# Optimization experiments

Measured on AMD Instinct MI355X. Metric: run time of the kernel, lower is better.

Reference implementation:

```python
import jax, jax.numpy as jnp
import numpy as np

B_, L_, D_ = 4, 4096, 256
EXPAND = 2
DI_ = EXPAND * D_      # 512 inner channels
H_ = 8                 # heads
P_ = DI_ // H_         # 64 head dim
N_ = 16                # d_state
K_ = 3                 # depthwise conv kernel


def setup_inputs() -> dict:
    key = jax.random.key(0)
    ks = jax.random.split(key, 32)

    def n(i, shape, s=0.02):
        return jax.random.normal(ks[i], shape, jnp.float32) * s

    inp = {"inputs": jax.random.normal(ks[0], (B_, L_, D_), jnp.float32)}
    i = 1
    for pre in ("f_", "b_"):
        inp[pre + "in_proj_w"] = n(i, (2 * DI_, D_)); i += 1
        inp[pre + "in_proj_b"] = jnp.zeros((2 * DI_,), jnp.float32)
        inp[pre + "x_proj_w"] = n(i, (DI_ + 2 * H_ * N_, DI_)); i += 1
        inp[pre + "x_proj_b"] = jnp.zeros((DI_ + 2 * H_ * N_,), jnp.float32)
        inp[pre + "dt_bias"] = jnp.full((DI_,), -4.0, jnp.float32)  # softplus -> small dt
        inp[pre + "A_log"] = jnp.log(jnp.tile(jnp.arange(1, N_ + 1, dtype=jnp.float32), (DI_, 1)))
        inp[pre + "D_skip"] = jnp.ones((DI_,), jnp.float32)
        inp[pre + "out_proj_w"] = n(i, (D_, DI_)); i += 1
        inp[pre + "out_proj_b"] = jnp.zeros((D_,), jnp.float32)
    inp["norm_w"] = jnp.ones((D_,), jnp.float32)
    inp["norm_b"] = jnp.zeros((D_,), jnp.float32)
    inp["conv_w"] = n(20, (D_, 1, K_), 0.1)   # depthwise: (out_ch, in_ch/groups=1, k)
    inp["conv_b"] = jnp.zeros((D_,), jnp.float32)
    return inp


def _layernorm(x, w, b):
    m = x.mean(-1, keepdims=True)
    v = ((x - m) ** 2).mean(-1, keepdims=True)
    return (x - m) * jax.lax.rsqrt(v + 1e-5) * w + b


def _mh_ssm(x, in_w, in_b, xp_w, xp_b, dt_b, A_log, D_skip, out_w, out_b):
    # Multihead selective-scan SSM (Mamba-style). x: (B, L, D)
    Bsz, L, _ = x.shape
    xz = x @ in_w.T + in_b                      # (B, L, 2*DI)
    xi, z = jnp.split(xz, 2, axis=-1)
    xi = jax.nn.silu(xi)                        # (B, L, DI)
    proj = xi @ xp_w.T + xp_b                   # (B, L, DI + 2*H*N)
    dt = jax.nn.softplus(proj[..., :DI_] + dt_b)        # (B, L, DI)
    Bm = proj[..., DI_:DI_ + H_ * N_].reshape(Bsz, L, H_, N_)
    Cm = proj[..., DI_ + H_ * N_:].reshape(Bsz, L, H_, N_)
    A = -jnp.exp(A_log).reshape(H_, P_, N_)     # (H, P, N), negative
    x4 = xi.reshape(Bsz, L, H_, P_)
    dt4 = dt.reshape(Bsz, L, H_, P_)

    def step(h, t):
        xt, dtt, Bt, Ct = t                     # (B,H,P), (B,H,P), (B,H,N), (B,H,N)
        dA = jnp.exp(dtt[..., None] * A)        # (B,H,P,N)
        h = h * dA + dtt[..., None] * Bt[:, :, None, :] * xt[..., None]
        y = jnp.einsum('bhpn,bhn->bhp', h, Ct)
        return h, y

    xs = (x4.transpose(1, 0, 2, 3), dt4.transpose(1, 0, 2, 3),
          Bm.transpose(1, 0, 2, 3), Cm.transpose(1, 0, 2, 3))
    h0 = jnp.zeros((Bsz, H_, P_, N_), x.dtype)
    _, ys = jax.lax.scan(step, h0, xs)          # ys: (L,B,H,P)
    y = ys.transpose(1, 0, 2, 3).reshape(Bsz, L, DI_) + xi * D_skip
    y = y * jax.nn.silu(z)                      # gating
    return y @ out_w.T + out_b                  # (B, L, D)


def reference(inputs,
              f_in_proj_w, f_in_proj_b, f_x_proj_w, f_x_proj_b, f_dt_bias,
              f_A_log, f_D_skip, f_out_proj_w, f_out_proj_b,
              b_in_proj_w, b_in_proj_b, b_x_proj_w, b_x_proj_b, b_dt_bias,
              b_A_log, b_D_skip, b_out_proj_w, b_out_proj_b,
              norm_w, norm_b, conv_w, conv_b):
    # Cascaded bidirectional SSM: backward(flip(norm(forward(x)))) then flip back
    y1 = _mh_ssm(inputs, f_in_proj_w, f_in_proj_b, f_x_proj_w, f_x_proj_b,
                 f_dt_bias, f_A_log, f_D_skip, f_out_proj_w, f_out_proj_b)
    y1n = jnp.flip(_layernorm(y1, norm_w, norm_b), axis=1)
    y2 = _mh_ssm(y1n, b_in_proj_w, b_in_proj_b, b_x_proj_w, b_x_proj_b,
                 b_dt_bias, b_A_log, b_D_skip, b_out_proj_w, b_out_proj_b)
    out = jnp.flip(y2, axis=1)
    # locality branch: depthwise Conv1d (groups=C) + exact GELU
    xt = inputs.transpose(0, 2, 1)              # (B, C, L)
    c = jax.lax.conv_general_dilated(
        xt, conv_w, window_strides=(1,), padding=[(1, 1)],
        dimension_numbers=('NCH', 'OIH', 'NCH'), feature_group_count=D_)
    c = jax.nn.gelu(c + conv_b[None, :, None], approximate=False)
    return out + c.transpose(0, 2, 1)
```

## Files before the change

kernel.cpp:

```cpp
#include <hip/hip_runtime.h>
#include <hip/hip_bf16.h>
#include <cstdint>
#include <cstddef>

#define B_  4
#define L_  4096
#define D_  256
#define DI_ 512
#define H_  8
#define P_  64
#define N_  16
#define M_  (B_ * L_)
#define PROJ_ (DI_ + 2 * H_ * N_)

#define NC_ 128
#define CL_ (L_ / NC_)
#define NSEQ_ (B_ * H_ * P_ * N_)
#define LOG2E_ 1.4426950408889634f

typedef __bf16 bf16x8 __attribute__((ext_vector_type(8)));
typedef float f32x4 __attribute__((ext_vector_type(4)));

__device__ __forceinline__ void cp16_lds(const __hip_bfloat16* g, short* lds) {
    __builtin_amdgcn_global_load_lds(
        (const __attribute__((address_space(1))) void*)g,
        (__attribute__((address_space(3))) void*)lds, 16, 0, 0);
}
__device__ __forceinline__ void cp16f_lds(const float* g, float* lds) {
    __builtin_amdgcn_global_load_lds(
        (const __attribute__((address_space(1))) void*)g,
        (__attribute__((address_space(3))) void*)lds, 16, 0, 0);
}

#define FS0 (M_ * D_)
#define FS1 (2 * DI_ * D_)
#define FS2 (PROJ_ * DI_)
#define FS3 (D_ * DI_)
#define FC1 (FS0 + FS1)
#define FC2 (FC1 + FS2)
#define FC3 (FC2 + FS3)
#define FC4 (FC3 + FS1)
#define FC5 (FC4 + FS2)
#define FC6 (FC5 + FS3)

__launch_bounds__(256)
__global__ void f2b_all(const float* __restrict__ i0, const float* __restrict__ i1,
                        const float* __restrict__ i2, const float* __restrict__ i3,
                        const float* __restrict__ i4, const float* __restrict__ i5,
                        const float* __restrict__ i6,
                        __hip_bfloat16* o0, __hip_bfloat16* o1, __hip_bfloat16* o2,
                        __hip_bfloat16* o3, __hip_bfloat16* o4, __hip_bfloat16* o5,
                        __hip_bfloat16* o6) {
    for (int idx = blockIdx.x * 256 + threadIdx.x; idx < FC6; idx += gridDim.x * 256) {
        const float* s; __hip_bfloat16* d; int off;
        if (idx < FS0)      { s = i0; d = o0; off = idx; }
        else if (idx < FC1) { s = i1; d = o1; off = idx - FS0; }
        else if (idx < FC2) { s = i2; d = o2; off = idx - FC1; }
        else if (idx < FC3) { s = i3; d = o3; off = idx - FC2; }
        else if (idx < FC4) { s = i4; d = o4; off = idx - FC3; }
        else if (idx < FC5) { s = i5; d = o5; off = idx - FC4; }
        else                { s = i6; d = o6; off = idx - FC5; }
        d[off] = __float2bfloat16(s[off]);
    }
}

template <int EPI>
__launch_bounds__(256)
__global__ void gemm_mfma(const __hip_bfloat16* __restrict__ A,
                          const __hip_bfloat16* __restrict__ W,
                          const float* __restrict__ bias, int Kv,
                          float* __restrict__ out0, float* __restrict__ out1,
                          __hip_bfloat16* __restrict__ obf,
                          const float* __restrict__ aux,
                          const float* __restrict__ cw,
                          const float* __restrict__ cb,
                          const float* __restrict__ cinp) {
    __shared__ short As[128 * 64];
    __shared__ short Bs[128 * 64];
    const int tid = threadIdx.x;
    const int lane = tid & 63;
    const int wave = tid >> 6;
    const int bm = blockIdx.x * 128;
    const int bn = blockIdx.y * 128;
    const int wm = (wave >> 1) * 64;
    const int wn = (wave & 1) * 64;

    f32x4 acc[4][4];
#pragma unroll
    for (int i = 0; i < 4; ++i)
#pragma unroll
        for (int j = 0; j < 4; ++j) acc[i][j] = (f32x4)0.f;

    const int srow = lane >> 3;
    const int ssegx = ((lane & 7) ^ srow) * 8;
    const __hip_bfloat16* gA0 = A + (size_t)(bm + wave * 32 + srow) * Kv + ssegx;
    const __hip_bfloat16* gB0 = W + (size_t)(bn + wave * 32 + srow) * Kv + ssegx;
    short* lA0 = As + (wave * 32) * 64;
    short* lB0 = Bs + (wave * 32) * 64;

    const int fr = lane & 15;
    const int kq = lane >> 4;

    for (int k0 = 0; k0 < Kv; k0 += 64) {
#pragma unroll
        for (int rb = 0; rb < 4; ++rb) {
            cp16_lds(gA0 + (size_t)(rb * 8) * Kv + k0, lA0 + rb * 8 * 64);
            cp16_lds(gB0 + (size_t)(rb * 8) * Kv + k0, lB0 + rb * 8 * 64);
        }
        __syncthreads();
#pragma unroll
        for (int ks = 0; ks < 2; ++ks) {
            const int kgg = ks * 4 + kq;
            const int kslot = (kgg ^ (fr & 7)) * 8;
            bf16x8 af[4], bv[4];
#pragma unroll
            for (int i = 0; i < 4; ++i)
                af[i] = *reinterpret_cast<const bf16x8*>(
                    &As[(wm + i * 16 + fr) * 64 + kslot]);
#pragma unroll
            for (int j = 0; j < 4; ++j)
                bv[j] = *reinterpret_cast<const bf16x8*>(
                    &Bs[(wn + j * 16 + fr) * 64 + kslot]);
#pragma unroll
            for (int i = 0; i < 4; ++i)
#pragma unroll
                for (int j = 0; j < 4; ++j)
                    acc[i][j] = __builtin_amdgcn_mfma_f32_16x16x32_bf16(
                        af[i], bv[j], acc[i][j], 0, 0, 0);
        }
        __syncthreads();
    }

    const int n16 = lane & 15;
    const int r4 = (lane >> 4) * 4;
#pragma unroll
    for (int i = 0; i < 4; ++i) {
#pragma unroll
        for (int j = 0; j < 4; ++j) {
            const int cg = bn + wn + j * 16 + n16;
            const float bb = bias[cg];
#pragma unroll
            for (int v = 0; v < 4; ++v) {
                const int r = bm + wm + i * 16 + r4 + v;
                float val = acc[i][j][v] + bb;
                if (EPI == 0) {
                    out0[(size_t)r * 256 + cg] = val;
                } else if (EPI == 1) {
                    if (cg < DI_) {
                        val = val / (1.f + __expf(-val));
                        obf[(size_t)r * DI_ + cg] = __float2bfloat16(val);
                    } else {
                        out1[(size_t)r * DI_ + cg - DI_] = val;
                    }
                } else if (EPI == 2) {
                    if (cg < DI_) {
                        const float x = val + aux[cg];
                        val = (x > 20.f) ? x : __logf(1.f + __expf(x));
                    }
                    out0[(size_t)r * PROJ_ + cg] = val;
                } else {
                    const int b = r >> 12;
                    const int l = r & (L_ - 1);
                    const int lo = L_ - 1 - l;
                    const size_t base = ((size_t)(b << 12) + lo) * 256 + cg;
                    float cv = fmaf(cinp[base], cw[cg * 3 + 1], cb[cg]);
                    if (lo > 0) cv = fmaf(cinp[base - 256], cw[cg * 3 + 0], cv);
                    if (lo + 1 < L_) cv = fmaf(cinp[base + 256], cw[cg * 3 + 2], cv);
                    const float g = 0.5f * cv * (1.f + erff(cv * 0.70710678118654752f));
                    out0[base] = val + g;
                }
            }
        }
    }
}


__device__ __forceinline__ bool a_is_arith(const float* A2) {
    bool ok = true;
#pragma unroll
    for (int n = 1; n < N_; ++n)
        ok = ok && (fabsf(A2[n] - (float)(n + 1) * A2[0]) <= 1e-4f * fabsf(A2[n]));
    return ok;
}

__launch_bounds__(256)
__global__ void scan_chunk_state(const __hip_bfloat16* __restrict__ xi,
                                 const float* __restrict__ proj,
                                 const float* __restrict__ A_log,
                                 float* __restrict__ st_prod,
                                 float* __restrict__ st_hend) {
    __shared__ float bsh[4][CL_][16];
    const int bh = blockIdx.x;
    const int b = bh >> 3;
    const int h = bh & 7;
    const int lane = threadIdx.x & 63;
    const int wave = threadIdx.x >> 6;
    const int chunk = blockIdx.y * 4 + wave;
    const int t0 = chunk * CL_;
    const int c = h * P_ + lane;
    const int bOff = DI_ + h * N_;

    {
        const int stp = lane >> 2;
        const int off4 = (lane & 3) * 4;
        const float* base = proj + ((size_t)b * L_ + t0) * PROJ_ + bOff + off4;
#pragma unroll
        for (int r = 0; r < 2; ++r)
            cp16f_lds(base + (size_t)(r * 16 + stp) * PROJ_,
                      &bsh[wave][0][0] + r * 256);
    }

    float A2[N_], hs[N_];
#pragma unroll
    for (int n = 0; n < N_; ++n) {
        A2[n] = -__expf(A_log[c * N_ + n]) * LOG2E_;
        hs[n] = 0.f;
    }
    const bool fast = a_is_arith(A2);
    __syncthreads();

    const float* pDt = proj + ((size_t)b * L_ + t0) * PROJ_ + c;
    const __hip_bfloat16* px = xi + ((size_t)b * L_ + t0) * DI_ + c;
    float S = 0.f;

    if (fast) {
        float dtb[2][4], xb[2][4];
#pragma unroll
        for (int i = 0; i < 4; ++i) {
            dtb[0][i] = pDt[(size_t)i * PROJ_];
            xb[0][i] = __bfloat162float(px[(size_t)i * DI_]);
        }
#pragma unroll
        for (int k = 0; k < CL_ / 4; ++k) {
            const int cur = k & 1, nxt = cur ^ 1;
            if (k + 1 < CL_ / 4) {
#pragma unroll
                for (int i = 0; i < 4; ++i) {
                    dtb[nxt][i] = pDt[(size_t)((k + 1) * 4 + i) * PROJ_];
                    xb[nxt][i] = __bfloat162float(px[(size_t)((k + 1) * 4 + i) * DI_]);
                }
            }
#pragma unroll
            for (int i = 0; i < 4; ++i) {
                const int t = k * 4 + i;
                const float dt_v = dtb[cur][i];
                const float dtx = dt_v * xb[cur][i];
                const float e1 = exp2f(dt_v * A2[0]);
                S += dt_v;
                const f32x4* bp = reinterpret_cast<const f32x4*>(&bsh[wave][t][0]);
                float dA = e1;
#pragma unroll
                for (int q = 0; q < 4; ++q) {
                    const f32x4 Bq = bp[q];
#pragma unroll
                    for (int j = 0; j < 4; ++j) {
                        hs[q * 4 + j] = fmaf(hs[q * 4 + j], dA, dtx * Bq[j]);
                        dA *= e1;
                    }
                }
            }
        }
    } else {
#pragma unroll 4
        for (int t = 0; t < CL_; ++t) {
            const float dt_v = pDt[(size_t)t * PROJ_];
            const float xv = __bfloat162float(px[(size_t)t * DI_]);
            const float dtx = dt_v * xv;
            S += dt_v;
#pragma unroll
            for (int n = 0; n < N_; ++n) {
                const float dA = exp2f(dt_v * A2[n]);
                hs[n] = fmaf(hs[n], dA, dtx * bsh[wave][t][n]);
            }
        }
    }

    const size_t s0 = (size_t)chunk * NSEQ_ + ((size_t)(bh * P_ + lane)) * N_;
#pragma unroll
    for (int n = 0; n < N_; n += 4) {
        *reinterpret_cast<float4*>(st_prod + s0 + n) =
            make_float4(exp2f(A2[n] * S), exp2f(A2[n + 1] * S),
                        exp2f(A2[n + 2] * S), exp2f(A2[n + 3] * S));
        *reinterpret_cast<float4*>(st_hend + s0 + n) =
            make_float4(hs[n], hs[n + 1], hs[n + 2], hs[n + 3]);
    }
}

__launch_bounds__(256)
__global__ void scan_combine(float* __restrict__ st_prod,
                             const float* __restrict__ st_hend) {
    const int s = blockIdx.x * 256 + threadIdx.x;
    float H = 0.f;
#pragma unroll 8
    for (int k = 0; k < NC_; ++k) {
        const size_t o = (size_t)k * NSEQ_ + s;
        const float Pv = st_prod[o];
        const float Ev = st_hend[o];
        st_prod[o] = H;
        H = fmaf(Pv, H, Ev);
    }
}

__launch_bounds__(256)
__global__ void scan_chunk_out(const __hip_bfloat16* __restrict__ xi,
                               const float* __restrict__ z,
                               const float* __restrict__ proj,
                               const float* __restrict__ A_log,
                               const float* __restrict__ D_skip,
                               const float* __restrict__ st_hin,
                               __hip_bfloat16* __restrict__ yg) {
    __shared__ float bc[4][CL_][32];
    const int bh = blockIdx.x;
    const int b = bh >> 3;
    const int h = bh & 7;
    const int lane = threadIdx.x & 63;
    const int wave = threadIdx.x >> 6;
    const int chunk = blockIdx.y * 4 + wave;
    const int t0 = chunk * CL_;
    const int c = h * P_ + lane;
    const int bOff = DI_ + h * N_;
    const int cOff = DI_ + H_ * N_ + h * N_;

    {
        const int seg = lane >> 2;
        const int off4 = (lane & 3) * 4;
        const float* rowb = proj + ((size_t)b * L_ + t0) * PROJ_;
#pragma unroll
        for (int r = 0; r < 4; ++r) {
            const int s = r * 16 + seg;
            const int stp = s >> 1;
            const int half = s & 1;
            cp16f_lds(rowb + (size_t)stp * PROJ_ + (half ? cOff : bOff) + off4,
                      &bc[wave][0][0] + r * 256);
        }
    }

    float A2[N_], hs[N_];
    const size_t s0 = (size_t)chunk * NSEQ_ + ((size_t)(bh * P_ + lane)) * N_;
#pragma unroll
    for (int n = 0; n < N_; n += 4) {
        const float4 h4 = *reinterpret_cast<const float4*>(st_hin + s0 + n);
        hs[n] = h4.x; hs[n + 1] = h4.y; hs[n + 2] = h4.z; hs[n + 3] = h4.w;
    }
#pragma unroll
    for (int n = 0; n < N_; ++n)
        A2[n] = -__expf(A_log[c * N_ + n]) * LOG2E_;
    const bool fast = a_is_arith(A2);
    const float Dv = D_skip[c];
    __syncthreads();

    const float* pDt = proj + ((size_t)b * L_ + t0) * PROJ_ + c;
    const __hip_bfloat16* px = xi + ((size_t)b * L_ + t0) * DI_ + c;
    const float* pz = z + ((size_t)b * L_ + t0) * DI_ + c;
    __hip_bfloat16* py = yg + ((size_t)b * L_ + t0) * DI_ + c;

    if (fast) {
        float dtb[2][4], xb[2][4], zb[2][4];
#pragma unroll
        for (int i = 0; i < 4; ++i) {
            dtb[0][i] = pDt[(size_t)i * PROJ_];
            xb[0][i] = __bfloat162float(px[(size_t)i * DI_]);
            zb[0][i] = pz[(size_t)i * DI_];
        }
#pragma unroll
        for (int k = 0; k < CL_ / 4; ++k) {
            const int cur = k & 1, nxt = cur ^ 1;
            if (k + 1 < CL_ / 4) {
#pragma unroll
                for (int i = 0; i < 4; ++i) {
                    const int t = (k + 1) * 4 + i;
                    dtb[nxt][i] = pDt[(size_t)t * PROJ_];
                    xb[nxt][i] = __bfloat162float(px[(size_t)t * DI_]);
                    zb[nxt][i] = pz[(size_t)t * DI_];
                }
            }
#pragma unroll
            for (int i = 0; i < 4; ++i) {
                const int t = k * 4 + i;
                const float dt_v = dtb[cur][i];
                const float xv = xb[cur][i];
                const float zv = zb[cur][i];
                const float dtx = dt_v * xv;
                const float e1 = exp2f(dt_v * A2[0]);
                const f32x4* bp = reinterpret_cast<const f32x4*>(&bc[wave][t][0]);
                float dA = e1;
                float y = 0.f;
#pragma unroll
                for (int q = 0; q < 4; ++q) {
                    const f32x4 Bq = bp[q];
                    const f32x4 Cq = bp[4 + q];
#pragma unroll
                    for (int j = 0; j < 4; ++j) {
                        hs[q * 4 + j] = fmaf(hs[q * 4 + j], dA, dtx * Bq[j]);
                        y = fmaf(hs[q * 4 + j], Cq[j], y);
                        dA *= e1;
                    }
                }
                const float g = zv / (1.f + __expf(-zv));
                py[(size_t)t * DI_] = __float2bfloat16((y + Dv * xv) * g);
            }
        }
    } else {
#pragma unroll 4
        for (int t = 0; t < CL_; ++t) {
            const float dt_v = pDt[(size_t)t * PROJ_];
            const float xv = __bfloat162float(px[(size_t)t * DI_]);
            const float zv = pz[(size_t)t * DI_];
            const float dtx = dt_v * xv;
            float y = 0.f;
#pragma unroll
            for (int n = 0; n < N_; ++n) {
                const float dA = exp2f(dt_v * A2[n]);
                hs[n] = fmaf(hs[n], dA, dtx * bc[wave][t][n]);
                y = fmaf(hs[n], bc[wave][t][16 + n], y);
            }
            const float g = zv / (1.f + __expf(-zv));
            py[(size_t)t * DI_] = __float2bfloat16((y + Dv * xv) * g);
        }
    }
}

__launch_bounds__(256)
__global__ void ln_flip(const float* __restrict__ x, const float* __restrict__ w,
                        const float* __restrict__ bvec, __hip_bfloat16* __restrict__ y) {
    const int row = blockIdx.x;
    const int d = threadIdx.x;
    const float v = x[(size_t)row * D_ + d];
    float s = v, s2 = v * v;
#pragma unroll
    for (int m = 32; m; m >>= 1) {
        s += __shfl_xor(s, m);
        s2 += __shfl_xor(s2, m);
    }
    __shared__ float sh[8];
    const int wave = d >> 6;
    if ((d & 63) == 0) { sh[wave] = s; sh[4 + wave] = s2; }
    __syncthreads();
    const float ts = sh[0] + sh[1] + sh[2] + sh[3];
    const float ts2 = sh[4] + sh[5] + sh[6] + sh[7];
    const float mean = ts * (1.f / D_);
    const float var = ts2 * (1.f / D_) - mean * mean;
    const float inv = rsqrtf(var + 1e-5f);
    const int b = row >> 12;
    const int l = row & (L_ - 1);
    const int drow = (b << 12) + (L_ - 1 - l);
    y[(size_t)drow * D_ + d] = __float2bfloat16((v - mean) * inv * w[d] + bvec[d]);
}

extern "C" void kernel_launch(void* const* d_in, const int* in_sizes, int n_in,
                              void* d_out, int out_size, void* d_ws, size_t ws_size,
                              hipStream_t stream) {
    const float* inputs = (const float*)d_in[0];
    const float* f_in_w = (const float*)d_in[1];
    const float* f_in_b = (const float*)d_in[2];
    const float* f_xp_w = (const float*)d_in[3];
    const float* f_xp_b = (const float*)d_in[4];
    const float* f_dt_b = (const float*)d_in[5];
    const float* f_A = (const float*)d_in[6];
    const float* f_D = (const float*)d_in[7];
    const float* f_out_w = (const float*)d_in[8];
    const float* f_out_b = (const float*)d_in[9];
    const float* b_in_w = (const float*)d_in[10];
    const float* b_in_b = (const float*)d_in[11];
    const float* b_xp_w = (const float*)d_in[12];
    const float* b_xp_b = (const float*)d_in[13];
    const float* b_dt_b = (const float*)d_in[14];
    const float* b_A = (const float*)d_in[15];
    const float* b_D = (const float*)d_in[16];
    const float* b_out_w = (const float*)d_in[17];
    const float* b_out_b = (const float*)d_in[18];
    const float* norm_w = (const float*)d_in[19];
    const float* norm_b = (const float*)d_in[20];
    const float* conv_w = (const float*)d_in[21];
    const float* conv_b = (const float*)d_in[22];
    float* out = (float*)d_out;

    float* ws = (float*)d_ws;
    float* st_prod = ws;
    float* st_hend = st_prod + (size_t)NSEQ_ * NC_;
    float* zbuf    = st_hend + (size_t)NSEQ_ * NC_;
    float* proj    = zbuf + (size_t)M_ * DI_;
    float* y1      = proj + (size_t)M_ * PROJ_;
    __hip_bfloat16* xi_bf = (__hip_bfloat16*)(y1 + (size_t)M_ * D_);
    __hip_bfloat16* yg_bf = xi_bf + (size_t)M_ * DI_;
    __hip_bfloat16* a_bf  = yg_bf + (size_t)M_ * DI_;
    __hip_bfloat16* wpool = a_bf + (size_t)M_ * D_;
    __hip_bfloat16* f_in_wb  = wpool;
    __hip_bfloat16* f_xp_wb  = f_in_wb + 2 * DI_ * D_;
    __hip_bfloat16* f_out_wb = f_xp_wb + PROJ_ * DI_;
    __hip_bfloat16* b_in_wb  = f_out_wb + D_ * DI_;
    __hip_bfloat16* b_xp_wb  = b_in_wb + 2 * DI_ * D_;
    __hip_bfloat16* b_out_wb = b_xp_wb + PROJ_ * DI_;

    const dim3 blk(256);
    const dim3 g_in(M_ / 128, (2 * DI_) / 128);
    const dim3 g_xp(M_ / 128, PROJ_ / 128);
    const dim3 g_out(M_ / 128, 2);
    const dim3 g_chunk(B_ * H_, NC_ / 4);
    const dim3 g_comb(NSEQ_ / 256);

    f2b_all<<<dim3(4096), blk, 0, stream>>>(inputs, f_in_w, f_xp_w, f_out_w,
                                            b_in_w, b_xp_w, b_out_w,
                                            a_bf, f_in_wb, f_xp_wb, f_out_wb,
                                            b_in_wb, b_xp_wb, b_out_wb);

    gemm_mfma<1><<<g_in, blk, 0, stream>>>(a_bf, f_in_wb, f_in_b, D_,
                                           nullptr, zbuf, xi_bf, nullptr,
                                           nullptr, nullptr, nullptr);
    gemm_mfma<2><<<g_xp, blk, 0, stream>>>(xi_bf, f_xp_wb, f_xp_b, DI_,
                                           proj, nullptr, nullptr, f_dt_b,
                                           nullptr, nullptr, nullptr);
    scan_chunk_state<<<g_chunk, blk, 0, stream>>>(xi_bf, proj, f_A, st_prod, st_hend);
    scan_combine<<<g_comb, blk, 0, stream>>>(st_prod, st_hend);
    scan_chunk_out<<<g_chunk, blk, 0, stream>>>(xi_bf, zbuf, proj, f_A, f_D,
                                                st_prod, yg_bf);
    gemm_mfma<0><<<g_out, blk, 0, stream>>>(yg_bf, f_out_wb, f_out_b, DI_,
                                            y1, nullptr, nullptr, nullptr,
                                            nullptr, nullptr, nullptr);
    ln_flip<<<dim3(M_), blk, 0, stream>>>(y1, norm_w, norm_b, a_bf);

    gemm_mfma<1><<<g_in, blk, 0, stream>>>(a_bf, b_in_wb, b_in_b, D_,
                                           nullptr, zbuf, xi_bf, nullptr,
                                           nullptr, nullptr, nullptr);
    gemm_mfma<2><<<g_xp, blk, 0, stream>>>(xi_bf, b_xp_wb, b_xp_b, DI_,
                                           proj, nullptr, nullptr, b_dt_b,
                                           nullptr, nullptr, nullptr);
    scan_chunk_state<<<g_chunk, blk, 0, stream>>>(xi_bf, proj, b_A, st_prod, st_hend);
    scan_combine<<<g_comb, blk, 0, stream>>>(st_prod, st_hend);
    scan_chunk_out<<<g_chunk, blk, 0, stream>>>(xi_bf, zbuf, proj, b_A, b_D,
                                                st_prod, yg_bf);
    gemm_mfma<3><<<g_out, blk, 0, stream>>>(yg_bf, b_out_wb, b_out_b, DI_,
                                            out, nullptr, nullptr, nullptr,
                                            conv_w, conv_b, inputs);
}
```

Before: 427.5 us.

## Fuse forward out-projection with LayerNorm+flip and store z gate in bf16

Adds a gemm_out_ln kernel in which each block computes 32 full rows of the 256-wide out-projection and then applies LayerNorm plus the sequence flip in the epilogue, writing bf16 directly. This removes the fp32 y1 round trip and the separate ln_flip launch. The z half of the in-projection is now stored as bf16 instead of fp32, halving that buffer's write and read traffic in the scan. The fused GEMM uses a 32-row tile (512 blocks) that reloads the full weight per block, and z loses precision.

```diff
diff --git a/kernel.cpp b/kernel.cpp
--- a/kernel.cpp
+++ b/kernel.cpp
@@ -69,7 +69,8 @@
 __global__ void gemm_mfma(const __hip_bfloat16* __restrict__ A,
                           const __hip_bfloat16* __restrict__ W,
                           const float* __restrict__ bias, int Kv,
-                          float* __restrict__ out0, float* __restrict__ out1,
+                          float* __restrict__ out0,
+                          __hip_bfloat16* __restrict__ zb,
                           __hip_bfloat16* __restrict__ obf,
                           const float* __restrict__ aux,
                           const float* __restrict__ cw,
@@ -143,14 +144,12 @@
             for (int v = 0; v < 4; ++v) {
                 const int r = bm + wm + i * 16 + r4 + v;
                 float val = acc[i][j][v] + bb;
-                if (EPI == 0) {
-                    out0[(size_t)r * 256 + cg] = val;
-                } else if (EPI == 1) {
+                if (EPI == 1) {
                     if (cg < DI_) {
                         val = val / (1.f + __expf(-val));
                         obf[(size_t)r * DI_ + cg] = __float2bfloat16(val);
                     } else {
-                        out1[(size_t)r * DI_ + cg - DI_] = val;
+                        zb[(size_t)r * DI_ + cg - DI_] = __float2bfloat16(val);
                     }
                 } else if (EPI == 2) {
                     if (cg < DI_) {
@@ -174,6 +173,122 @@
     }
 }
 
+__launch_bounds__(256)
+__global__ void gemm_out_ln(const __hip_bfloat16* __restrict__ A,
+                            const __hip_bfloat16* __restrict__ W,
+                            const float* __restrict__ bias,
+                            const float* __restrict__ lnw,
+                            const float* __restrict__ lnb,
+                            __hip_bfloat16* __restrict__ outb) {
+    __shared__ short As[32 * 64];
+    __shared__ short Ws[256 * 64];
+    __shared__ float rs[2][4][32];
+    const int tid = threadIdx.x;
+    const int lane = tid & 63;
+    const int wave = tid >> 6;
+    const int bm = blockIdx.x * 32;
+    const int Kv = DI_;
+
+    f32x4 acc[2][4];
+#pragma unroll
+    for (int i = 0; i < 2; ++i)
+#pragma unroll
+        for (int j = 0; j < 4; ++j) acc[i][j] = (f32x4)0.f;
+
+    const int srow = lane >> 3;
+    const int ssegx = ((lane & 7) ^ srow) * 8;
+    const __hip_bfloat16* gA0 = A + (size_t)(bm + wave * 8 + srow) * Kv + ssegx;
+    const __hip_bfloat16* gW0 = W + (size_t)(wave * 64 + srow) * Kv + ssegx;
+    short* lA0 = As + (wave * 8) * 64;
+    short* lW0 = Ws + (wave * 64) * 64;
+
+    const int fr = lane & 15;
+    const int kq = lane >> 4;
+
+    for (int k0 = 0; k0 < Kv; k0 += 64) {
+        cp16_lds(gA0 + k0, lA0);
+#pragma unroll
+        for (int rb = 0; rb < 8; ++rb)
+            cp16_lds(gW0 + (size_t)(rb * 8) * Kv + k0, lW0 + rb * 8 * 64);
+        __syncthreads();
+#pragma unroll
+        for (int ks = 0; ks < 2; ++ks) {
+            const int kgg = ks * 4 + kq;
+            const int kslot = (kgg ^ (fr & 7)) * 8;
+            bf16x8 af[2], bv[4];
+#pragma unroll
+            for (int i = 0; i < 2; ++i)
+                af[i] = *reinterpret_cast<const bf16x8*>(
+                    &As[(i * 16 + fr) * 64 + kslot]);
+#pragma unroll
+            for (int j = 0; j < 4; ++j)
+                bv[j] = *reinterpret_cast<const bf16x8*>(
+                    &Ws[(wave * 64 + j * 16 + fr) * 64 + kslot]);
+#pragma unroll
+            for (int i = 0; i < 2; ++i)
+#pragma unroll
+                for (int j = 0; j < 4; ++j)
+                    acc[i][j] = __builtin_amdgcn_mfma_f32_16x16x32_bf16(
+                        af[i], bv[j], acc[i][j], 0, 0, 0);
+        }
+        __syncthreads();
+    }
+
+    const int n16 = lane & 15;
+    const int r4 = (lane >> 4) * 4;
+    float vals[2][4][4];
+#pragma unroll
+    for (int i = 0; i < 2; ++i)
+#pragma unroll
+        for (int j = 0; j < 4; ++j) {
+            const float bb = bias[wave * 64 + j * 16 + n16];
+#pragma unroll
+            for (int v = 0; v < 4; ++v) vals[i][j][v] = acc[i][j][v] + bb;
+        }
+
+#pragma unroll
+    for (int i = 0; i < 2; ++i)
+#pragma unroll
+        for (int v = 0; v < 4; ++v) {
+            float s = 0.f, s2 = 0.f;
+#pragma unroll
+            for (int j = 0; j < 4; ++j) {
+                const float t = vals[i][j][v];
+                s += t; s2 = fmaf(t, t, s2);
+            }
+            s += __shfl_xor(s, 1); s2 += __shfl_xor(s2, 1);
+            s += __shfl_xor(s, 2); s2 += __shfl_xor(s2, 2);
+            s += __shfl_xor(s, 4); s2 += __shfl_xor(s2, 4);
+            s += __shfl_xor(s, 8); s2 += __shfl_xor(s2, 8);
+            if (n16 == 0) {
+                rs[0][wave][i * 16 + r4 + v] = s;
+                rs[1][wave][i * 16 + r4 + v] = s2;
+            }
+        }
+    __syncthreads();
+
+#pragma unroll
+    for (int i = 0; i < 2; ++i)
+#pragma unroll
+        for (int v = 0; v < 4; ++v) {
+            const int row = i * 16 + r4 + v;
+            const float ts = rs[0][0][row] + rs[0][1][row] + rs[0][2][row] + rs[0][3][row];
+            const float ts2 = rs[1][0][row] + rs[1][1][row] + rs[1][2][row] + rs[1][3][row];
+            const float mean = ts * (1.f / 256.f);
+            const float var = ts2 * (1.f / 256.f) - mean * mean;
+            const float inv = rsqrtf(var + 1e-5f);
+            const int rg = bm + row;
+            const int b = rg >> 12;
+            const int l = rg & (L_ - 1);
+            const size_t drow = (size_t)((b << 12) + (L_ - 1 - l)) * 256;
+#pragma unroll
+            for (int j = 0; j < 4; ++j) {
+                const int cg = wave * 64 + j * 16 + n16;
+                const float o = (vals[i][j][v] - mean) * inv * lnw[cg] + lnb[cg];
+                outb[drow + cg] = __float2bfloat16(o);
+            }
+        }
+}
 
 __device__ __forceinline__ bool a_is_arith(const float* A2) {
     bool ok = true;
@@ -303,7 +418,7 @@
 
 __launch_bounds__(256)
 __global__ void scan_chunk_out(const __hip_bfloat16* __restrict__ xi,
-                               const float* __restrict__ z,
+                               const __hip_bfloat16* __restrict__ z,
                                const float* __restrict__ proj,
                                const float* __restrict__ A_log,
                                const float* __restrict__ D_skip,
@@ -351,7 +466,7 @@
 
     const float* pDt = proj + ((size_t)b * L_ + t0) * PROJ_ + c;
     const __hip_bfloat16* px = xi + ((size_t)b * L_ + t0) * DI_ + c;
-    const float* pz = z + ((size_t)b * L_ + t0) * DI_ + c;
+    const __hip_bfloat16* pz = z + ((size_t)b * L_ + t0) * DI_ + c;
     __hip_bfloat16* py = yg + ((size_t)b * L_ + t0) * DI_ + c;
 
     if (fast) {
@@ -360,7 +475,7 @@
         for (int i = 0; i < 4; ++i) {
             dtb[0][i] = pDt[(size_t)i * PROJ_];
             xb[0][i] = __bfloat162float(px[(size_t)i * DI_]);
-            zb[0][i] = pz[(size_t)i * DI_];
+            zb[0][i] = __bfloat162float(pz[(size_t)i * DI_]);
         }
 #pragma unroll
         for (int k = 0; k < CL_ / 4; ++k) {
@@ -371,7 +486,7 @@
                     const int t = (k + 1) * 4 + i;
                     dtb[nxt][i] = pDt[(size_t)t * PROJ_];
                     xb[nxt][i] = __bfloat162float(px[(size_t)t * DI_]);
-                    zb[nxt][i] = pz[(size_t)t * DI_];
+                    zb[nxt][i] = __bfloat162float(pz[(size_t)t * DI_]);
                 }
             }
 #pragma unroll
@@ -405,7 +520,7 @@
         for (int t = 0; t < CL_; ++t) {
             const float dt_v = pDt[(size_t)t * PROJ_];
             const float xv = __bfloat162float(px[(size_t)t * DI_]);
-            const float zv = pz[(size_t)t * DI_];
+            const float zv = __bfloat162float(pz[(size_t)t * DI_]);
             const float dtx = dt_v * xv;
             float y = 0.f;
 #pragma unroll
@@ -418,33 +533,6 @@
             py[(size_t)t * DI_] = __float2bfloat16((y + Dv * xv) * g);
         }
     }
-}
-
-__launch_bounds__(256)
-__global__ void ln_flip(const float* __restrict__ x, const float* __restrict__ w,
-                        const float* __restrict__ bvec, __hip_bfloat16* __restrict__ y) {
-    const int row = blockIdx.x;
-    const int d = threadIdx.x;
-    const float v = x[(size_t)row * D_ + d];
-    float s = v, s2 = v * v;
-#pragma unroll
-    for (int m = 32; m; m >>= 1) {
-        s += __shfl_xor(s, m);
-        s2 += __shfl_xor(s2, m);
-    }
-    __shared__ float sh[8];
-    const int wave = d >> 6;
-    if ((d & 63) == 0) { sh[wave] = s; sh[4 + wave] = s2; }
-    __syncthreads();
-    const float ts = sh[0] + sh[1] + sh[2] + sh[3];
-    const float ts2 = sh[4] + sh[5] + sh[6] + sh[7];
-    const float mean = ts * (1.f / D_);
-    const float var = ts2 * (1.f / D_) - mean * mean;
-    const float inv = rsqrtf(var + 1e-5f);
-    const int b = row >> 12;
-    const int l = row & (L_ - 1);
-    const int drow = (b << 12) + (L_ - 1 - l);
-    y[(size_t)drow * D_ + d] = __float2bfloat16((v - mean) * inv * w[d] + bvec[d]);
 }
 
 extern "C" void kernel_launch(void* const* d_in, const int* in_sizes, int n_in,
@@ -478,8 +566,9 @@
     float* ws = (float*)d_ws;
     float* st_prod = ws;
     float* st_hend = st_prod + (size_t)NSEQ_ * NC_;
-    float* zbuf    = st_hend + (size_t)NSEQ_ * NC_;
-    float* proj    = zbuf + (size_t)M_ * DI_;
+    float* zslot   = st_hend + (size_t)NSEQ_ * NC_;
+    __hip_bfloat16* z_bf = (__hip_bfloat16*)zslot;
+    float* proj    = zslot + (size_t)M_ * DI_;
     float* y1      = proj + (size_t)M_ * PROJ_;
     __hip_bfloat16* xi_bf = (__hip_bfloat16*)(y1 + (size_t)M_ * D_);
     __hip_bfloat16* yg_bf = xi_bf + (size_t)M_ * DI_;
@@ -496,6 +585,7 @@
     const dim3 g_in(M_ / 128, (2 * DI_) / 128);
     const dim3 g_xp(M_ / 128, PROJ_ / 128);
     const dim3 g_out(M_ / 128, 2);
+    const dim3 g_oln(M_ / 32);
     const dim3 g_chunk(B_ * H_, NC_ / 4);
     const dim3 g_comb(NSEQ_ / 256);
 
@@ -505,29 +595,27 @@
                                             b_in_wb, b_xp_wb, b_out_wb);
 
     gemm_mfma<1><<<g_in, blk, 0, stream>>>(a_bf, f_in_wb, f_in_b, D_,
-                                           nullptr, zbuf, xi_bf, nullptr,
+                                           nullptr, z_bf, xi_bf, nullptr,
                                            nullptr, nullptr, nullptr);
     gemm_mfma<2><<<g_xp, blk, 0, stream>>>(xi_bf, f_xp_wb, f_xp_b, DI_,
                                            proj, nullptr, nullptr, f_dt_b,
                                            nullptr, nullptr, nullptr);
     scan_chunk_state<<<g_chunk, blk, 0, stream>>>(xi_bf, proj, f_A, st_prod, st_hend);
     scan_combine<<<g_comb, blk, 0, stream>>>(st_prod, st_hend);
-    scan_chunk_out<<<g_chunk, blk, 0, stream>>>(xi_bf, zbuf, proj, f_A, f_D,
+    scan_chunk_out<<<g_chunk, blk, 0, stream>>>(xi_bf, z_bf, proj, f_A, f_D,
                                                 st_prod, yg_bf);
-    gemm_mfma<0><<<g_out, blk, 0, stream>>>(yg_bf, f_out_wb, f_out_b, DI_,
-                                            y1, nullptr, nullptr, nullptr,
-                                            nullptr, nullptr, nullptr);
-    ln_flip<<<dim3(M_), blk, 0, stream>>>(y1, norm_w, norm_b, a_bf);
+    gemm_out_ln<<<g_oln, blk, 0, stream>>>(yg_bf, f_out_wb, f_out_b,
+                                           norm_w, norm_b, a_bf);
 
     gemm_mfma<1><<<g_in, blk, 0, stream>>>(a_bf, b_in_wb, b_in_b, D_,
-                                           nullptr, zbuf, xi_bf, nullptr,
+                                           nullptr, z_bf, xi_bf, nullptr,
                                            nullptr, nullptr, nullptr);
     gemm_mfma<2><<<g_xp, blk, 0, stream>>>(xi_bf, b_xp_wb, b_xp_b, DI_,
                                            proj, nullptr, nullptr, b_dt_b,
                                            nullptr, nullptr, nullptr);
     scan_chunk_state<<<g_chunk, blk, 0, stream>>>(xi_bf, proj, b_A, st_prod, st_hend);
     scan_combine<<<g_comb, blk, 0, stream>>>(st_prod, st_hend);
-    scan_chunk_out<<<g_chunk, blk, 0, stream>>>(xi_bf, zbuf, proj, b_A, b_D,
+    scan_chunk_out<<<g_chunk, blk, 0, stream>>>(xi_bf, z_bf, proj, b_A, b_D,
                                                 st_prod, yg_bf);
     gemm_mfma<3><<<g_out, blk, 0, stream>>>(yg_bf, b_out_wb, b_out_b, DI_,
                                             out, nullptr, nullptr, nullptr,
```

Measured after the change: 399.9 us. 1.07x faster.
